# Kernel tuning notes

Measured on AMD Instinct MI355X. Metric: run time of the kernel, lower is better.

The kernel has to match this reference:

```python
import jax, jax.numpy as jnp
import numpy as np

D = 200; K = 10; NHEAD = 5; HDIM = 40; ANS = 2; THRESH = 0.4; GHEAD = 5; GC = 2
B = 8; L = 80; R = 64

def _lin(x, W, b):
    return x @ W + b

def _ln(x, g, b):
    m = jnp.mean(x, -1, keepdims=True)
    v = jnp.var(x, -1, keepdims=True)
    return (x - m) / jnp.sqrt(v + 1e-5) * g + b

def _sparsemax(z):
    # sparsemax along last axis (Martins & Astudillo)
    zs = -jnp.sort(-z, axis=-1)
    k = jnp.arange(1, z.shape[-1] + 1, dtype=z.dtype)
    cs = jnp.cumsum(zs, -1)
    supp = jnp.sum((1.0 + k * zs) > cs, -1, keepdims=True)
    tau = (jnp.take_along_axis(cs, supp - 1, -1) - 1.0) / supp.astype(z.dtype)
    return jnp.maximum(z - tau, 0.0)

def _pair(a, b):
    # a [B,n,d], b [B,m,d] -> [B,n*m,4d] feature cat [a, b, a*b, a-b]
    Bn, n, d = a.shape; m = b.shape[1]
    a1 = jnp.broadcast_to(a[:, :, None, :], (Bn, n, m, d))
    b1 = jnp.broadcast_to(b[:, None, :, :], (Bn, n, m, d))
    return jnp.concatenate([a1, b1, a1 * b1, a1 - b1], -1).reshape(Bn, n * m, 4 * d)

def _topk_sel(E, s, mask):
    # select top-K instances by score (masked)
    s = jnp.where(mask, s, -jnp.inf)
    _, idx = jax.lax.top_k(s, K)
    return jnp.take_along_axis(E, idx[:, :, None], axis=1)

def _mco(x, W_attn, b_attn, W_ff1, b_ff1, W_ff2, b_ff2, ln_g, ln_b):
    # transformer encoder layer: MHA + FFN, post-norm (dropout off at eval)
    Bn, N, d = x.shape
    q = _lin(x, W_attn[0], b_attn[0]).reshape(Bn, N, NHEAD, HDIM)
    k = _lin(x, W_attn[1], b_attn[1]).reshape(Bn, N, NHEAD, HDIM)
    v = _lin(x, W_attn[2], b_attn[2]).reshape(Bn, N, NHEAD, HDIM)
    att = jax.nn.softmax(jnp.einsum('bnhk,bmhk->bhnm', q, k) / np.float32(np.sqrt(HDIM)), axis=-1)
    o = jnp.einsum('bhnm,bmhk->bnhk', att, v).reshape(Bn, N, d)
    x = _ln(x + _lin(o, W_attn[3], b_attn[3]), ln_g[0], ln_b[0])
    f = _lin(jax.nn.relu(_lin(x, W_ff1, b_ff1)), W_ff2, b_ff2)
    return _ln(x + f, ln_g[1], ln_b[1])

def _forward(imgs, encoded_texts, mask_T, mask_TT, mask_TV, adj,
             answer_set, Wt, bt, Wi1, bi1, Wi2, bi2, Wgc, bgc, Wps, bps, Wts, bts,
             W_single, b_single, W_pair1, b_pair1, W_pair2, b_pair2, W_topk, b_topk,
             clues, W_clue1, b_clue1, W_ans1, b_ans1, W_inst2, b_inst2, W_ans2, b_ans2,
             W_attn, b_attn, W_ff1, b_ff1, W_ff2, b_ff2, ln_g, ln_b,
             W_guide, b_guide, W_at1, b_at1, W_at2, b_at2):
    imgs_0 = jax.nn.relu(_lin(jax.nn.relu(_lin(imgs, Wi1, bi1)), Wi2, bi2))  # ImageEncoder 768->500->200
    texts_0 = _lin(encoded_texts, Wt, bt)                                    # TextEncoder 768->200
    Bn, l, _ = texts_0.shape
    r = imgs_0.shape[1]
    ones_V = jnp.ones((Bn, r), bool)
    ones_VV = jnp.ones((Bn, r * r), bool)
    out = []
    for gc_i in range(GC):
        def pair_mlp(f, i):
            return jax.nn.relu(_lin(jax.nn.relu(_lin(f, W_pair1[i], b_pair1[i])), W_pair2[i], b_pair2[i]))
        def score(E, i):
            return jax.nn.relu(E @ W_topk[i] + b_topk[i])
        # five modality streams
        E_T = jax.nn.relu(_lin(texts_0, W_single[0], b_single[0]))
        E_V = jax.nn.relu(_lin(imgs_0, W_single[1], b_single[1]))
        E_TT = pair_mlp(_pair(texts_0, texts_0), 0)
        E_TV = pair_mlp(_pair(texts_0, imgs_0), 1)
        E_VV = pair_mlp(_pair(imgs_0, imgs_0), 2)
        E_T_k = _topk_sel(E_T, score(E_T, 0), mask_T)
        E_V_k = _topk_sel(E_V, score(E_V, 1), ones_V)
        E_TT_k = _topk_sel(E_TT, score(E_TT, 2), mask_TT)
        E_TV_k = _topk_sel(E_TV, score(E_TV, 3), mask_TV)
        E_VV_k = _topk_sel(E_VV, score(E_VV, 4), ones_VV)
        # clue binding: attend selected instances onto per-stream clue banks, condition on answer set
        ans1 = _lin(answer_set, W_ans1, b_ans1)
        def bind(Ek, c):
            att = jax.nn.softmax(jnp.einsum('bkd,cd->bkc', Ek, c), -1)
            bound = jnp.einsum('bkc,cd->bkd', att, c)
            return jax.nn.relu(_lin(bound, W_clue1, b_clue1)[:, :, None, :] + ans1[None, None])
        preds = jnp.concatenate([bind(E_T_k, clues[0]), bind(E_V_k, clues[1]), bind(E_TT_k, clues[2]), bind(E_TV_k, clues[3]), bind(E_VV_k, clues[4])], axis=1)  # [B,5K,A,D]
        E_cat = jnp.concatenate([E_T_k, E_V_k, E_TT_k, E_TV_k, E_VV_k], 1)
        E4 = jnp.broadcast_to(E_cat[:, :, None, :], preds.shape)
        inst_score = jnp.einsum('bnad,ad->bna', _lin(E4, W_inst2, b_inst2), _lin(answer_set, W_ans2, b_ans2))
        preds_ = jnp.stack([_mco(preds[:, :, a, :], W_attn, b_attn, W_ff1, b_ff1, W_ff2, b_ff2, ln_g, ln_b) for a in range(ANS)], axis=2)
        feat = jnp.concatenate([E4, preds, E4 - preds, E4 * preds], -1)
        atoms = jax.nn.sigmoid(_lin(jax.nn.relu(_lin(feat, W_at1, b_at1)), W_at2, b_at2))[..., 0]
        atoms = jnp.transpose(atoms, (2, 0, 1))  # [A,B,5K]
        # global text/image embeddings for guide scores
        I_score = jax.nn.softmax(imgs_0 @ Wps + bps, -1)
        T_score = jax.nn.softmax(texts_0 @ Wts + bts, -1)
        I_emb = jnp.einsum('brd,br->bd', imgs_0, I_score)
        T_emb = jnp.einsum('bld,bl->bd', texts_0, T_score)
        E_IT = pair_mlp(jnp.concatenate([T_emb, I_emb, T_emb * I_emb, T_emb - I_emb], -1), 1)
        heads = []
        for gi in range(GHEAD):
            g1 = jnp.einsum('bnad,d->bna', preds_, W_guide[2 * gi]) + b_guide[2 * gi]
            g2 = (E_IT @ W_guide[2 * gi + 1] + b_guide[2 * gi + 1])[:, None, None]
            fcs = _sparsemax(g1 * g2) * _sparsemax(inst_score)
            fcs = _sparsemax(jnp.transpose(fcs, (2, 0, 1)))  # [A,B,5K], sparsemax over instances
            flag = fcs >= THRESH
            mprod = jnp.prod(jnp.where(flag, atoms, 1.0), -1)  # conjunction over selected atoms
            vals, idx = jax.lax.top_k(fcs, 3)                  # fallback: top-3 atoms weighted by score
            fb = jnp.prod(jnp.take_along_axis(atoms, idx, -1) * vals, -1)
            heads.append(jnp.where(jnp.any(flag, -1), mprod, fb))  # [A,B]
        out.append(jnp.max(jnp.stack(heads, -1), -1))  # max over guide heads -> [A,B]
        # graph convolution refines text+image node features for next iteration
        graph = jnp.concatenate([texts_0, imgs_0], 1)
        graph = jax.nn.relu(jnp.einsum('bnm,bmd->bnd', adj, graph) @ Wgc[gc_i] + bgc[gc_i])
        texts_0 = graph[:, :l, :]
        imgs_0 = graph[:, l:, :]
    return jnp.stack(out)  # [GC, A, B]

def setup_inputs():
    ks = jax.random.split(jax.random.key(0), 64)
    def rn(i, shape, s=0.05):
        return jax.random.normal(ks[i], shape, dtype=jnp.float32) * s
    inp = {}
    inp['imgs'] = rn(0, (B, R, 768), 1.0)
    inp['encoded_texts'] = rn(1, (B, L, 768), 1.0)
    inp['mask_batch_T'] = jnp.ones((B, L), dtype=bool)
    inp['mask_batch_TT'] = jnp.ones((B, L * L), dtype=bool)
    inp['mask_batch_TV'] = jnp.ones((B, L * R), dtype=bool)
    inp['adj_matrix'] = jax.random.uniform(ks[2], (B, L + R, L + R), dtype=jnp.float32) / (L + R)
    inp['word_len'] = jax.random.randint(ks[3], (B,), 1, L)
    inp['word_spans'] = jax.random.randint(ks[4], (B, L, 2), 0, L)
    inp['answer_set'] = rn(5, (ANS, D), 0.5)
    inp['Wt'] = rn(6, (768, D)); inp['bt'] = rn(7, (D,))
    inp['Wi1'] = rn(8, (768, 500)); inp['bi1'] = rn(9, (500,))
    inp['Wi2'] = rn(10, (500, D)); inp['bi2'] = rn(11, (D,))
    inp['Wgc'] = rn(12, (GC, D, D)); inp['bgc'] = rn(13, (GC, D))
    inp['Wps'] = rn(14, (D,), 0.5); inp['bps'] = rn(15, ())
    inp['Wts'] = rn(16, (D,), 0.5); inp['bts'] = rn(17, ())
    inp['W_single'] = rn(18, (2, D, D)); inp['b_single'] = rn(19, (2, D))
    inp['W_pair1'] = rn(20, (3, 4 * D, 2 * D)); inp['b_pair1'] = rn(21, (3, 2 * D))
    inp['W_pair2'] = rn(22, (3, 2 * D, D)); inp['b_pair2'] = rn(23, (3, D))
    inp['W_topk'] = rn(24, (5, D), 0.5); inp['b_topk'] = rn(25, (5,))
    inp['clues'] = rn(26, (5, 5, D), 0.5)
    inp['W_clue1'] = rn(27, (D, D)); inp['b_clue1'] = rn(28, (D,))
    inp['W_ans1'] = rn(29, (D, D)); inp['b_ans1'] = rn(30, (D,))
    inp['W_inst2'] = rn(31, (D, D)); inp['b_inst2'] = rn(32, (D,))
    inp['W_ans2'] = rn(33, (D, D)); inp['b_ans2'] = rn(34, (D,))
    inp['W_attn'] = rn(35, (4, D, D)); inp['b_attn'] = rn(36, (4, D))
    inp['W_ff1'] = rn(37, (D, 2 * D)); inp['b_ff1'] = rn(38, (2 * D,))
    inp['W_ff2'] = rn(39, (2 * D, D)); inp['b_ff2'] = rn(40, (D,))
    inp['ln_g'] = jnp.ones((2, D), jnp.float32); inp['ln_b'] = jnp.zeros((2, D), jnp.float32)
    inp['W_guide'] = rn(41, (2 * GHEAD, D), 0.5); inp['b_guide'] = rn(42, (2 * GHEAD,))
    inp['W_at1'] = rn(43, (4 * D, 2 * D)); inp['b_at1'] = rn(44, (2 * D,))
    inp['W_at2'] = rn(45, (2 * D, 1)); inp['b_at2'] = rn(46, (1,))
    return inp

def reference(imgs, encoded_texts, mask_batch_T, mask_batch_TT, mask_batch_TV, adj_matrix, word_len, word_spans,
              answer_set, Wt, bt, Wi1, bi1, Wi2, bi2, Wgc, bgc, Wps, bps, Wts, bts,
              W_single, b_single, W_pair1, b_pair1, W_pair2, b_pair2, W_topk, b_topk,
              clues, W_clue1, b_clue1, W_ans1, b_ans1, W_inst2, b_inst2, W_ans2, b_ans2,
              W_attn, b_attn, W_ff1, b_ff1, W_ff2, b_ff2, ln_g, ln_b,
              W_guide, b_guide, W_at1, b_at1, W_at2, b_at2):
    # word_len / word_spans are consumed by the (simplified) TextEncoder pooling; not needed here
    return _forward(imgs, encoded_texts, mask_batch_T, mask_batch_TT, mask_batch_TV, adj_matrix,
                    answer_set, Wt, bt, Wi1, bi1, Wi2, bi2, Wgc, bgc, Wps, bps, Wts, bts,
                    W_single, b_single, W_pair1, b_pair1, W_pair2, b_pair2, W_topk, b_topk,
                    clues, W_clue1, b_clue1, W_ans1, b_ans1, W_inst2, b_inst2, W_ans2, b_ans2,
                    W_attn, b_attn, W_ff1, b_ff1, W_ff2, b_ff2, ln_g, ln_b,
                    W_guide, b_guide, W_at1, b_at1, W_at2, b_at2)
```

## Files before the change

kernel.cpp:

```cpp
#include <hip/hip_runtime.h>
#include <hip/hip_bf16.h>


__device__ __forceinline__ void sparsemax2(float z0, float z1, float& o0, float& o1) {
  float S0 = (z1 > z0) ? z1 : 0.f;
  float S1 = (z0 > z1) ? z0 : 0.f;
  float cz0 = (z1 > z0) ? z0 : 0.f;
  float cz1 = (z0 > z1) ? z1 : 0.f;
  bool c0 = (1.f + cz0) > S0;
  bool c1 = (1.f + cz1) > S1;
  float supp = (c0 ? 1.f : 0.f) + (c1 ? 1.f : 0.f);
  float Ss   = (c0 ? z0  : 0.f) + (c1 ? z1  : 0.f);
  float tau = (Ss - 1.f) / supp;
  o0 = fmaxf(z0 - tau, 0.f);
  o1 = fmaxf(z1 - tau, 0.f);
}

__global__ __launch_bounds__(256) void gemm_k(
    const float* __restrict__ A, const float* __restrict__ Bw,
    const float* __restrict__ bias, float* __restrict__ C,
    int M, int N, int K, long sA, long sB, long sC, int act)
{
  int batch = blockIdx.z;
  A  += (long)batch * sA;
  Bw += (long)batch * sB;
  C  += (long)batch * sC;
  __shared__ float As[32][33];
  __shared__ float Bs[32][33];
  int tid = threadIdx.x;
  int tx = tid & 15, ty = tid >> 4;
  int row0 = blockIdx.y * 32, col0 = blockIdx.x * 32;
  float acc00 = 0.f, acc01 = 0.f, acc10 = 0.f, acc11 = 0.f;
  for (int k0 = 0; k0 < K; k0 += 32) {
    for (int i = tid; i < 1024; i += 256) {
      int r = i >> 5, c = i & 31;
      int ar = row0 + r, ac = k0 + c;
      As[r][c] = (ar < M && ac < K) ? A[(long)ar * K + ac] : 0.f;
      int br = k0 + r, bc = col0 + c;
      Bs[r][c] = (br < K && bc < N) ? Bw[(long)br * N + bc] : 0.f;
    }
    __syncthreads();
#pragma unroll
    for (int kk = 0; kk < 32; ++kk) {
      float a0 = As[ty * 2][kk], a1 = As[ty * 2 + 1][kk];
      float b0 = Bs[kk][tx * 2], b1 = Bs[kk][tx * 2 + 1];
      acc00 += a0 * b0; acc01 += a0 * b1; acc10 += a1 * b0; acc11 += a1 * b1;
    }
    __syncthreads();
  }
  int r0 = row0 + ty * 2, c0 = col0 + tx * 2;
#define STORE_(rr, cc, v)                                        \
  if ((rr) < M && (cc) < N) {                                    \
    float t_ = (v) + (bias ? bias[cc] : 0.f);                    \
    if (act) t_ = fmaxf(t_, 0.f);                                \
    C[(long)(rr) * N + (cc)] = t_;                               \
  }
  STORE_(r0, c0, acc00); STORE_(r0, c0 + 1, acc01);
  STORE_(r0 + 1, c0, acc10); STORE_(r0 + 1, c0 + 1, acc11);
#undef STORE_
}

__global__ void wab_kernel(const float* __restrict__ P1, float* __restrict__ Wa,
                           float* __restrict__ Wb) {
  int idx = blockIdx.x * 256 + threadIdx.x;
  if (idx >= 240000) return;
  int t = idx / 80000, r2 = idx % 80000;
  int d = r2 / 400, k = r2 % 400;
  long base = (long)t * 320000;
  float wd = P1[base + (long)(600 + d) * 400 + k];
  Wa[idx] = P1[base + (long)d * 400 + k] + wd;
  Wb[idx] = P1[base + (long)(200 + d) * 400 + k] - wd;
}

__global__ void repack_kernel(const float* __restrict__ W_pair1,
                              const float* __restrict__ W_pair2,
                              float* __restrict__ Wcq, float* __restrict__ W2q) {
  int idx = blockIdx.x * 256 + threadIdx.x;
  if (idx < 259200) {
    int t = idx / 86400, r = idx % 86400;
    int dc = r / 1728, r2 = r % 1728;
    int tk = r2 / 108, m = r2 % 108;
    int j = m >> 2, dd = m & 3;
    const float* Wc = W_pair1 + (long)t * 320000 + 160000;
    Wcq[idx] = (j < 25) ? Wc[(long)(dc * 4 + dd) * 400 + tk * 25 + j] : 0.f;
  } else if (idx < 518400) {
    int id2 = idx - 259200;
    int t = id2 / 86400, r = id2 % 86400;
    int kc = r / 864, r2 = r % 864;
    int c8 = r2 / 108, m = r2 % 108;
    int j = m >> 2, kk = m & 3;
    const float* W2 = W_pair2 + (long)t * 80000;
    W2q[id2] = (j < 25) ? W2[(long)(kc * 4 + kk) * 200 + c8 * 25 + j] : 0.f;
  }
}

__global__ void ans_kernel(const float* __restrict__ as, const float* __restrict__ W1,
                           const float* __restrict__ b1, const float* __restrict__ W2,
                           const float* __restrict__ b2, float* __restrict__ ans1,
                           float* __restrict__ ans2) {
  int idx = blockIdx.x * 256 + threadIdx.x;
  if (idx >= 400) return;
  int a = idx / 200, d = idx % 200;
  float a1 = b1[d], a2 = b2[d];
  for (int k = 0; k < 200; ++k) {
    float av = as[a * 200 + k];
    a1 += av * W1[k * 200 + d];
    a2 += av * W2[k * 200 + d];
  }
  ans1[idx] = a1;
  ans2[idx] = a2;
}

__global__ void rowdot_kernel(const float* __restrict__ E, const float* __restrict__ Wt,
                              const float* __restrict__ bt, int g, float* __restrict__ s,
                              int rows) {
  int r = blockIdx.x * 256 + threadIdx.x;
  if (r >= rows) return;
  const float* e = E + (long)r * 200;
  const float* w = Wt + g * 200;
  float acc = bt[g];
  for (int d = 0; d < 200; ++d) acc += e[d] * w[d];
  s[r] = fmaxf(acc, 0.f);
}

__global__ __launch_bounds__(256) void pair_score_kernel(
    const float* __restrict__ Arows, int an, const float* __restrict__ Brows, int bm,
    const float* __restrict__ At, const float* __restrict__ Bt,
    const float* __restrict__ Wcq, const float* __restrict__ W2q,
    const float* __restrict__ b2, const float* __restrict__ wt,
    const float* __restrict__ btk, int gidx, float* __restrict__ scores)
{
  const int tid = threadIdx.x;
  const int b = blockIdx.y;
  const int nTJ = bm >> 2;
  const int i0 = (blockIdx.x / nTJ) * 8;
  const int j0 = (blockIdx.x % nTJ) * 4;

  Arows += (long)b * an * 200;
  Brows += (long)b * bm * 200;
  At += (long)b * an * 400;
  Bt += (long)b * bm * 400;
  scores += (long)b * an * bm;

  __shared__ __align__(16) float smem[12800];
  __shared__ __align__(16) float stg[3456];

  const int tq = tid >> 4;
  const int tk = tid & 15;
  const int tp8 = tid >> 3;
  const int tc8 = tid & 7;

  for (int idx = tid; idx < 6400; idx += 256) {
    int p = idx / 200, d = idx - p * 200;
    smem[p * 200 + d] = Arows[(long)(i0 + (p >> 2)) * 200 + d] *
                        Brows[(long)(j0 + (p & 3)) * 200 + d];
  }

  {
    const float4* src = reinterpret_cast<const float4*>(Wcq);
    float4* dst = reinterpret_cast<float4*>(stg);
#pragma unroll
    for (int l = 0; l < 2; ++l) {
      int idx = tid + l * 256;
      if (idx < 432) dst[idx] = src[idx];
    }
  }
  __syncthreads();

  float acc[2][25];
#pragma unroll
  for (int q = 0; q < 2; ++q)
#pragma unroll
    for (int j = 0; j < 25; ++j) acc[q][j] = 0.f;

  for (int ph = 0; ph < 50; ++ph) {
    const int cur = ph & 1, nxt = cur ^ 1;
    float4 pre[2];
    if (ph < 49) {
      const float4* src = reinterpret_cast<const float4*>(Wcq) + (ph + 1) * 432;
#pragma unroll
      for (int l = 0; l < 2; ++l) {
        int idx = tid + l * 256;
        pre[l] = (idx < 432) ? src[idx] : make_float4(0.f, 0.f, 0.f, 0.f);
      }
    }
    const float4* pd4 = reinterpret_cast<const float4*>(smem);
    const float4 p0 = pd4[(2 * tq + 0) * 50 + ph];
    const float4 p1 = pd4[(2 * tq + 1) * 50 + ph];
    const float4* wb = reinterpret_cast<const float4*>(stg) + cur * 432 + tk * 27;
#pragma unroll
    for (int j = 0; j < 25; ++j) {
      const float4 w = wb[j];
      float a0 = acc[0][j], a1 = acc[1][j];
      a0 = fmaf(p0.x, w.x, a0); a1 = fmaf(p1.x, w.x, a1);
      a0 = fmaf(p0.y, w.y, a0); a1 = fmaf(p1.y, w.y, a1);
      a0 = fmaf(p0.z, w.z, a0); a1 = fmaf(p1.z, w.z, a1);
      a0 = fmaf(p0.w, w.w, a0); a1 = fmaf(p1.w, w.w, a1);
      acc[0][j] = a0; acc[1][j] = a1;
    }
    if (ph < 49) {
      float4* dst = reinterpret_cast<float4*>(stg) + nxt * 432;
#pragma unroll
      for (int l = 0; l < 2; ++l) {
        int idx = tid + l * 256;
        if (idx < 432) dst[idx] = pre[l];
      }
    }
    __syncthreads();
  }

  {
    const float* Ar = &At[(long)(i0 + (tq >> 1)) * 400 + tk * 25];
#pragma unroll
    for (int q = 0; q < 2; ++q) {
      const float* Br = &Bt[(long)(j0 + ((2 * tq + q) & 3)) * 400 + tk * 25];
#pragma unroll
      for (int j = 0; j < 25; ++j)
        acc[q][j] = fmaxf(acc[q][j] + Ar[j] + Br[j], 0.f);
    }
  }

#pragma unroll
  for (int q = 0; q < 2; ++q)
#pragma unroll
    for (int j = 0; j < 25; ++j)
      smem[(2 * tq + q) * 400 + tk * 25 + j] = acc[q][j];
  {
    const float4* src = reinterpret_cast<const float4*>(W2q);
    float4* dst = reinterpret_cast<float4*>(stg);
#pragma unroll
    for (int l = 0; l < 2; ++l) {
      int idx = tid + l * 256;
      if (idx < 432) dst[idx] = src[idx];
    }
  }
  __syncthreads();

  float acc2[25];
#pragma unroll
  for (int j = 0; j < 25; ++j) acc2[j] = 0.f;

  for (int ph = 0; ph < 50; ++ph) {
    const int cur = ph & 1, nxt = cur ^ 1;
    float4 pre[2];
    if (ph < 49) {
      const float4* src = reinterpret_cast<const float4*>(W2q) + (ph + 1) * 432;
#pragma unroll
      for (int l = 0; l < 2; ++l) {
        int idx = tid + l * 256;
        pre[l] = (idx < 432) ? src[idx] : make_float4(0.f, 0.f, 0.f, 0.f);
      }
    }
    const float4* H4 = reinterpret_cast<const float4*>(smem);
#pragma unroll
    for (int gg = 0; gg < 2; ++gg) {
      const int kc = ph * 2 + gg;
      const float4 h = H4[tp8 * 100 + kc];
      const float4* wb =
          reinterpret_cast<const float4*>(stg) + cur * 432 + gg * 216 + tc8 * 27;
#pragma unroll
      for (int j = 0; j < 25; ++j) {
        const float4 w = wb[j];
        float a = acc2[j];
        a = fmaf(h.x, w.x, a);
        a = fmaf(h.y, w.y, a);
        a = fmaf(h.z, w.z, a);
        a = fmaf(h.w, w.w, a);
        acc2[j] = a;
      }
    }
    if (ph < 49) {
      float4* dst = reinterpret_cast<float4*>(stg) + nxt * 432;
#pragma unroll
      for (int l = 0; l < 2; ++l) {
        int idx = tid + l * 256;
        if (idx < 432) dst[idx] = pre[l];
      }
    }
    __syncthreads();
  }

  float part = 0.f;
#pragma unroll
  for (int j = 0; j < 25; ++j) {
    const int c = tc8 * 25 + j;
    part += fmaxf(acc2[j] + b2[c], 0.f) * wt[c];
  }
#pragma unroll
  for (int off = 1; off < 8; off <<= 1) part += __shfl_xor(part, off, 64);
  if ((tid & 7) == 0) {
    const int p = tp8;
    scores[(long)(i0 + (p >> 2)) * bm + (j0 + (p & 3))] =
        fmaxf(part + btk[gidx], 0.f);
  }
}

__global__ void topk_kernel(const float* __restrict__ sT, const float* __restrict__ sV,
                            const float* __restrict__ sTT, const float* __restrict__ sTV,
                            const float* __restrict__ sVV, int* __restrict__ topIdx) {
  int g = blockIdx.x, b = blockIdx.y, tid = threadIdx.x;
  const float* src; int len;
  switch (g) {
    case 0: src = sT + b * 80; len = 80; break;
    case 1: src = sV + b * 64; len = 64; break;
    case 2: src = sTT + b * 6400; len = 6400; break;
    case 3: src = sTV + b * 5120; len = 5120; break;
    default: src = sVV + b * 4096; len = 4096; break;
  }
  __shared__ float sbuf[6400];
  __shared__ float rv[256];
  __shared__ int ri[256];
  for (int i = tid; i < len; i += 256) sbuf[i] = src[i];
  __syncthreads();
  for (int r = 0; r < 10; ++r) {
    float bv = -1e30f; int bi = 0x7fffffff;
    for (int i = tid; i < len; i += 256) {
      float v = sbuf[i];
      if (v > bv) { bv = v; bi = i; }
    }
    rv[tid] = bv; ri[tid] = bi;
    __syncthreads();
    for (int s = 128; s > 0; s >>= 1) {
      if (tid < s) {
        if (rv[tid + s] > rv[tid] || (rv[tid + s] == rv[tid] && ri[tid + s] < ri[tid])) {
          rv[tid] = rv[tid + s]; ri[tid] = ri[tid + s];
        }
      }
      __syncthreads();
    }
    if (tid == 0) {
      topIdx[(g * 8 + b) * 10 + r] = ri[0];
      sbuf[ri[0]] = -1e30f;
    }
    __syncthreads();
  }
}

__global__ void gather_kernel(
    const int* __restrict__ topIdx, const float* __restrict__ ETf,
    const float* __restrict__ EVf, const float* __restrict__ texts0,
    const float* __restrict__ imgs0, const float* __restrict__ AtTT,
    const float* __restrict__ BtTT, const float* __restrict__ AtTV,
    const float* __restrict__ BtTV, const float* __restrict__ AtVV,
    const float* __restrict__ BtVV, const float* __restrict__ W_pair1,
    const float* __restrict__ W_pair2, const float* __restrict__ b_pair2,
    float* __restrict__ E_cat)
{
  int n = blockIdx.x, b = blockIdx.y, tid = threadIdx.x;
  int g = n / 10, r = n % 10;
  int idx = topIdx[(g * 8 + b) * 10 + r];
  float* out = E_cat + ((long)(b * 50 + n)) * 200;
  if (g == 0) {
    for (int d = tid; d < 200; d += 256) out[d] = ETf[((long)(b * 80 + idx)) * 200 + d];
    return;
  }
  if (g == 1) {
    for (int d = tid; d < 200; d += 256) out[d] = EVf[((long)(b * 64 + idx)) * 200 + d];
    return;
  }
  int t = g - 2;
  int m = (t == 0) ? 80 : 64;
  int i = idx / m, j = idx % m;
  const float* ar = (t == 2) ? imgs0 + ((long)(b * 64 + i)) * 200
                             : texts0 + ((long)(b * 80 + i)) * 200;
  const float* br = (t == 0) ? texts0 + ((long)(b * 80 + j)) * 200
                             : imgs0 + ((long)(b * 64 + j)) * 200;
  const float* Atp = ((t == 0) ? AtTT : (t == 1) ? AtTV : AtVV) +
                     ((long)(b * ((t == 2) ? 64 : 80) + i)) * 400;
  const float* Btp = ((t == 0) ? BtTT : (t == 1) ? BtTV : BtVV) +
                     ((long)(b * ((t == 0) ? 80 : 64) + j)) * 400;
  const float* Wc = W_pair1 + (long)t * 320000 + 160000;
  const float* W2 = W_pair2 + (long)t * 80000;
  const float* bb2 = b_pair2 + t * 200;
  __shared__ float pd[200];
  __shared__ float hh[400];
  for (int d = tid; d < 200; d += 256) pd[d] = ar[d] * br[d];
  __syncthreads();
  for (int k = tid; k < 400; k += 256) {
    float acc = Atp[k] + Btp[k];
    for (int d = 0; d < 200; ++d) acc += pd[d] * Wc[(long)d * 400 + k];
    hh[k] = fmaxf(acc, 0.f);
  }
  __syncthreads();
  for (int c = tid; c < 200; c += 256) {
    float acc = bb2[c];
    for (int k = 0; k < 400; ++k) acc += hh[k] * W2[(long)k * 200 + c];
    out[c] = fmaxf(acc, 0.f);
  }
}

__global__ void bind_kernel(const float* __restrict__ E_cat, const float* __restrict__ clues,
                            const float* __restrict__ W_clue1, const float* __restrict__ b_clue1,
                            const float* __restrict__ ans1, const float* __restrict__ W_inst2,
                            const float* __restrict__ b_inst2, const float* __restrict__ ans2,
                            float* __restrict__ preds, float* __restrict__ inst) {
  int n = blockIdx.x, b = blockIdx.y, tid = threadIdx.x;
  int g = n / 10;
  const float* e = E_cat + ((long)(b * 50 + n)) * 200;
  __shared__ float es[200], att[5], bound[200], vv[200], red[256];
  for (int d = tid; d < 200; d += 256) es[d] = e[d];
  __syncthreads();
  if (tid < 5) {
    const float* cl = clues + ((long)(g * 5 + tid)) * 200;
    float acc = 0.f;
    for (int d = 0; d < 200; ++d) acc += es[d] * cl[d];
    att[tid] = acc;
  }
  __syncthreads();
  if (tid == 0) {
    float mx = att[0];
    for (int c = 1; c < 5; ++c) mx = fmaxf(mx, att[c]);
    float s = 0.f;
    for (int c = 0; c < 5; ++c) { att[c] = expf(att[c] - mx); s += att[c]; }
    float inv = 1.f / s;
    for (int c = 0; c < 5; ++c) att[c] *= inv;
  }
  __syncthreads();
  if (tid < 200) {
    float acc = 0.f;
    for (int c = 0; c < 5; ++c) acc += att[c] * clues[((long)(g * 5 + c)) * 200 + tid];
    bound[tid] = acc;
  }
  __syncthreads();
  if (tid < 200) {
    float acc = b_clue1[tid];
    for (int k = 0; k < 200; ++k) acc += bound[k] * W_clue1[(long)k * 200 + tid];
    long rbase = ((long)(b * 50 + n)) * 2;
    preds[(rbase + 0) * 200 + tid] = fmaxf(acc + ans1[tid], 0.f);
    preds[(rbase + 1) * 200 + tid] = fmaxf(acc + ans1[200 + tid], 0.f);
    float a2 = b_inst2[tid];
    for (int k = 0; k < 200; ++k) a2 += es[k] * W_inst2[(long)k * 200 + tid];
    vv[tid] = a2;
  }
  __syncthreads();
  float p0 = 0.f, p1 = 0.f;
  for (int d = tid; d < 200; d += 256) {
    p0 += vv[d] * ans2[d];
    p1 += vv[d] * ans2[200 + d];
  }
  red[tid] = p0; __syncthreads();
  for (int s = 128; s > 0; s >>= 1) { if (tid < s) red[tid] += red[tid + s]; __syncthreads(); }
  if (tid == 0) inst[((long)(b * 50 + n)) * 2 + 0] = red[0];
  __syncthreads();
  red[tid] = p1; __syncthreads();
  for (int s = 128; s > 0; s >>= 1) { if (tid < s) red[tid] += red[tid + s]; __syncthreads(); }
  if (tid == 0) inst[((long)(b * 50 + n)) * 2 + 1] = red[0];
// ... 200 lines not shown
    }
    __syncthreads();
    if (tid < 100) {
      int a = tid / 50, n = tid % 50;
      fcs[a][n] = fmaxf(fcs1[n][a] - tau[a], 0.f);
    }
    __syncthreads();
    if (tid < 2) {
      int a = tid;
      bool anyF = false;
      float mp = 1.f;
      for (int n = 0; n < 50; ++n) {
        if (fcs[a][n] >= 0.4f) { anyF = true; mp *= atm[n][a]; }
      }
      int p0 = -1, p1 = -1;
      float fb = 1.f;
      for (int t3 = 0; t3 < 3; ++t3) {
        float bv = -1e30f; int bi = -1;
        for (int n = 0; n < 50; ++n) {
          if (n == p0 || n == p1) continue;
          float v = fcs[a][n];
          if (v > bv) { bv = v; bi = n; }
        }
        if (t3 == 0) p0 = bi; else if (t3 == 1) p1 = bi;
        fb *= atm[bi][a] * bv;
      }
      float head = anyF ? mp : fb;
      hm[a] = fmaxf(hm[a], head);
    }
    __syncthreads();
  }
  if (tid < 2) dout[gc * 16 + tid * 8 + b] = hm[tid];
}

__global__ void graph_pack(const float* __restrict__ texts0, const float* __restrict__ imgs0,
                           float* __restrict__ gin) {
  int row = blockIdx.x, tid = threadIdx.x;
  int b = row / 144, rr = row % 144;
  const float* src = (rr < 80) ? texts0 + ((long)(b * 80 + rr)) * 200
                               : imgs0 + ((long)(b * 64 + rr - 80)) * 200;
  float* dst = gin + (long)row * 200;
  if (tid < 200) dst[tid] = src[tid];
}

__global__ void graph_unpack(const float* __restrict__ gout, float* __restrict__ texts0,
                             float* __restrict__ imgs0) {
  int row = blockIdx.x, tid = threadIdx.x;
  int b = row / 144, rr = row % 144;
  const float* src = gout + (long)row * 200;
  float* dst = (rr < 80) ? texts0 + ((long)(b * 80 + rr)) * 200
                         : imgs0 + ((long)(b * 64 + rr - 80)) * 200;
  if (tid < 200) dst[tid] = src[tid];
}

extern "C" void kernel_launch(void* const* d_in, const int* in_sizes, int n_in,
                              void* d_out, int out_size, void* d_ws, size_t ws_size,
                              hipStream_t stream) {
  (void)in_sizes; (void)n_in; (void)out_size; (void)ws_size;
  const float* imgs = (const float*)d_in[0];
  const float* etexts = (const float*)d_in[1];
  const float* adj = (const float*)d_in[5];
  const float* answer_set = (const float*)d_in[8];
  const float* Wt = (const float*)d_in[9];
  const float* bt = (const float*)d_in[10];
  const float* Wi1 = (const float*)d_in[11];
  const float* bi1 = (const float*)d_in[12];
  const float* Wi2 = (const float*)d_in[13];
  const float* bi2 = (const float*)d_in[14];
  const float* Wgc = (const float*)d_in[15];
  const float* bgc = (const float*)d_in[16];
  const float* Wps = (const float*)d_in[17];
  const float* bps = (const float*)d_in[18];
  const float* Wts = (const float*)d_in[19];
  const float* bts = (const float*)d_in[20];
  const float* W_single = (const float*)d_in[21];
  const float* b_single = (const float*)d_in[22];
  const float* W_pair1 = (const float*)d_in[23];
  const float* b_pair1 = (const float*)d_in[24];
  const float* W_pair2 = (const float*)d_in[25];
  const float* b_pair2 = (const float*)d_in[26];
  const float* W_topk = (const float*)d_in[27];
  const float* b_topk = (const float*)d_in[28];
  const float* clues = (const float*)d_in[29];
  const float* W_clue1 = (const float*)d_in[30];
  const float* b_clue1 = (const float*)d_in[31];
  const float* W_ans1 = (const float*)d_in[32];
  const float* b_ans1 = (const float*)d_in[33];
  const float* W_inst2 = (const float*)d_in[34];
  const float* b_inst2 = (const float*)d_in[35];
  const float* W_ans2 = (const float*)d_in[36];
  const float* b_ans2 = (const float*)d_in[37];
  const float* W_attn = (const float*)d_in[38];
  const float* b_attn = (const float*)d_in[39];
  const float* W_ff1 = (const float*)d_in[40];
  const float* b_ff1 = (const float*)d_in[41];
  const float* W_ff2 = (const float*)d_in[42];
  const float* b_ff2 = (const float*)d_in[43];
  const float* ln_g = (const float*)d_in[44];
  const float* ln_b = (const float*)d_in[45];
  const float* W_guide = (const float*)d_in[46];
  const float* b_guide = (const float*)d_in[47];
  const float* W_at1 = (const float*)d_in[48];
  const float* b_at1 = (const float*)d_in[49];
  const float* W_at2 = (const float*)d_in[50];
  const float* b_at2 = (const float*)d_in[51];

  float* W = (float*)d_ws;
  size_t off = 0;
  auto A_ = [&](size_t n) { float* p = W + off; off += n; return p; };
  float* texts0 = A_(128000);
  float* imgs0 = A_(102400);
  float* tmp500 = A_(256000);
  float* Wa = A_(240000);
  float* Wb = A_(240000);
  float* Wcq = A_(259200);
  float* W2q = A_(259200);
  float* AtTT = A_(256000);
  float* BtTT = A_(256000);
  float* AtTV = A_(256000);
  float* BtTV = A_(204800);
  float* AtVV = A_(204800);
  float* BtVV = A_(204800);
  float* ETf = A_(128000);
  float* EVf = A_(102400);
  float* sT = A_(640);
  float* sV = A_(512);
  float* sTT = A_(51200);
  float* sTV = A_(40960);
  float* sVV = A_(32768);
  float* E_cat = A_(80000);
  float* ans1 = A_(400);
  float* ans2 = A_(400);
  float* preds = A_(160000);
  float* inst = A_(800);
  float* bufQ = A_(160000);
  float* bufK = A_(160000);
  float* bufV = A_(160000);
  float* bufO = A_(160000);
  float* bufT1 = A_(160000);
  float* bufX1 = A_(160000);
  float* bufF1 = A_(320000);
  float* bufF2 = A_(160000);
  float* predsM = A_(160000);
  float* featb = A_(640000);
  float* bufAt = A_(320000);
  float* atoms = A_(800);
  float* E_IT = A_(1600);
  float* gin = A_(230400);
  float* tmpG = A_(230400);
  float* gout = A_(230400);
  int* topIdx = (int*)A_(400);

  dim3 blk(256);
  auto launch_gemm = [&](const float* Aa, const float* Bb, const float* bias, float* C,
                         int M, int N, int K, int act, int batch = 1, long sA = 0,
                         long sB = 0, long sC = 0) {
    dim3 g((N + 31) / 32, (M + 31) / 32, batch);
    gemm_k<<<g, blk, 0, stream>>>(Aa, Bb, bias, C, M, N, K, sA, sB, sC, act);
  };

  launch_gemm(imgs, Wi1, bi1, tmp500, 512, 500, 768, 1);
  launch_gemm(tmp500, Wi2, bi2, imgs0, 512, 200, 500, 1);
  launch_gemm(etexts, Wt, bt, texts0, 640, 200, 768, 0);
  wab_kernel<<<(240000 + 255) / 256, blk, 0, stream>>>(W_pair1, Wa, Wb);
  repack_kernel<<<(518400 + 255) / 256, blk, 0, stream>>>(W_pair1, W_pair2, Wcq, W2q);
  ans_kernel<<<2, blk, 0, stream>>>(answer_set, W_ans1, b_ans1, W_ans2, b_ans2, ans1, ans2);

  for (int gc = 0; gc < 2; ++gc) {
    launch_gemm(texts0, W_single, b_single, ETf, 640, 200, 200, 1);
    launch_gemm(imgs0, W_single + 40000, b_single + 200, EVf, 512, 200, 200, 1);
    rowdot_kernel<<<3, blk, 0, stream>>>(ETf, W_topk, b_topk, 0, sT, 640);
    rowdot_kernel<<<2, blk, 0, stream>>>(EVf, W_topk, b_topk, 1, sV, 512);
    launch_gemm(texts0, Wa, nullptr, AtTT, 640, 400, 200, 0);
    launch_gemm(texts0, Wb, b_pair1, BtTT, 640, 400, 200, 0);
    launch_gemm(texts0, Wa + 80000, nullptr, AtTV, 640, 400, 200, 0);
    launch_gemm(imgs0, Wb + 80000, b_pair1 + 400, BtTV, 512, 400, 200, 0);
    launch_gemm(imgs0, Wa + 160000, nullptr, AtVV, 512, 400, 200, 0);
    launch_gemm(imgs0, Wb + 160000, b_pair1 + 800, BtVV, 512, 400, 200, 0);
    pair_score_kernel<<<dim3(200, 8), blk, 0, stream>>>(
        texts0, 80, texts0, 80, AtTT, BtTT, Wcq, W2q, b_pair2,
        W_topk + 400, b_topk, 2, sTT);
    pair_score_kernel<<<dim3(160, 8), blk, 0, stream>>>(
        texts0, 80, imgs0, 64, AtTV, BtTV, Wcq + 86400, W2q + 86400,
        b_pair2 + 200, W_topk + 600, b_topk, 3, sTV);
    pair_score_kernel<<<dim3(128, 8), blk, 0, stream>>>(
        imgs0, 64, imgs0, 64, AtVV, BtVV, Wcq + 172800, W2q + 172800,
        b_pair2 + 400, W_topk + 800, b_topk, 4, sVV);
    topk_kernel<<<dim3(5, 8), blk, 0, stream>>>(sT, sV, sTT, sTV, sVV, topIdx);
    gather_kernel<<<dim3(50, 8), blk, 0, stream>>>(topIdx, ETf, EVf, texts0, imgs0, AtTT,
                                                   BtTT, AtTV, BtTV, AtVV, BtVV, W_pair1,
                                                   W_pair2, b_pair2, E_cat);
    bind_kernel<<<dim3(50, 8), blk, 0, stream>>>(E_cat, clues, W_clue1, b_clue1, ans1,
                                                 W_inst2, b_inst2, ans2, preds, inst);
    launch_gemm(preds, W_attn, b_attn, bufQ, 800, 200, 200, 0);
    launch_gemm(preds, W_attn + 40000, b_attn + 200, bufK, 800, 200, 200, 0);
    launch_gemm(preds, W_attn + 80000, b_attn + 400, bufV, 800, 200, 200, 0);
    attn_kernel<<<dim3(5, 2, 8), blk, 0, stream>>>(bufQ, bufK, bufV, bufO);
    launch_gemm(bufO, W_attn + 120000, b_attn + 600, bufT1, 800, 200, 200, 0);
    ln_kernel<<<800, blk, 0, stream>>>(preds, bufT1, ln_g, ln_b, bufX1);
    launch_gemm(bufX1, W_ff1, b_ff1, bufF1, 800, 400, 200, 1);
    launch_gemm(bufF1, W_ff2, b_ff2, bufF2, 800, 200, 400, 0);
    ln_kernel<<<800, blk, 0, stream>>>(bufX1, bufF2, ln_g + 200, ln_b + 200, predsM);
    feat_kernel<<<800, blk, 0, stream>>>(E_cat, preds, featb);
    launch_gemm(featb, W_at1, b_at1, bufAt, 800, 400, 800, 1);
    atoms_kernel<<<800, blk, 0, stream>>>(bufAt, W_at2, b_at2, atoms);
    emb_kernel<<<8, blk, 0, stream>>>(texts0, imgs0, Wts, bts, Wps, bps, W_pair1, b_pair1,
                                      W_pair2, b_pair2, E_IT);
    head_kernel<<<8, blk, 0, stream>>>(predsM, inst, atoms, E_IT, W_guide, b_guide,
                                       (float*)d_out, gc);
    if (gc == 0) {
      graph_pack<<<1152, blk, 0, stream>>>(texts0, imgs0, gin);
      launch_gemm(adj, gin, nullptr, tmpG, 144, 200, 144, 0, 8, 144 * 144, 144 * 200,
                  144 * 200);
      launch_gemm(tmpG, Wgc, bgc, gout, 1152, 200, 200, 1);
      graph_unpack<<<1152, blk, 0, stream>>>(gout, texts0, imgs0);
    }
  }
}
```

Before: 4.712 ms.

## Double pair tile per block in pair_score and split second GEMM into halves

Each pair_score block now handles 8x8 pairs instead of 8x4. Every thread accumulates four pair rows in the first GEMM and two in the second, so each staged weight element is reused across twice as many pairs, and the grid is halved. The hidden activations are written to shared memory in two swizzled halves so that the 64-pair by 400 hidden tile fits in the existing buffer. The cost is higher register pressure (acc grows to 100 floats), which may reduce occupancy or spill, and fewer blocks to fill the GPU.

```diff
diff --git a/kernel.cpp b/kernel.cpp
--- a/kernel.cpp
+++ b/kernel.cpp
@@ -132,9 +132,9 @@
 {
   const int tid = threadIdx.x;
   const int b = blockIdx.y;
-  const int nTJ = bm >> 2;
+  const int nTJ = bm >> 3;
   const int i0 = (blockIdx.x / nTJ) * 8;
-  const int j0 = (blockIdx.x % nTJ) * 4;
+  const int j0 = (blockIdx.x % nTJ) * 8;
 
   Arows += (long)b * an * 200;
   Brows += (long)b * bm * 200;
@@ -145,153 +145,164 @@
   __shared__ __align__(16) float smem[12800];
   __shared__ __align__(16) float stg[3456];
 
-  const int tq = tid >> 4;
+  const int tp = tid >> 4;
   const int tk = tid & 15;
-  const int tp8 = tid >> 3;
+  const int u = tid >> 3;
   const int tc8 = tid & 7;
 
-  for (int idx = tid; idx < 6400; idx += 256) {
+  for (int idx = tid; idx < 12800; idx += 256) {
     int p = idx / 200, d = idx - p * 200;
-    smem[p * 200 + d] = Arows[(long)(i0 + (p >> 2)) * 200 + d] *
-                        Brows[(long)(j0 + (p & 3)) * 200 + d];
+    smem[p * 200 + d] = Arows[(long)(i0 + (p >> 3)) * 200 + d] *
+                        Brows[(long)(j0 + (p & 7)) * 200 + d];
   }
 
   {
     const float4* src = reinterpret_cast<const float4*>(Wcq);
     float4* dst = reinterpret_cast<float4*>(stg);
-#pragma unroll
-    for (int l = 0; l < 2; ++l) {
-      int idx = tid + l * 256;
-      if (idx < 432) dst[idx] = src[idx];
-    }
-  }
-  __syncthreads();
-
-  float acc[2][25];
-#pragma unroll
-  for (int q = 0; q < 2; ++q)
+    dst[tid] = src[tid];
+    if (tid < 176) dst[256 + tid] = src[256 + tid];
+  }
+  __syncthreads();
+
+  float acc[4][25];
+#pragma unroll
+  for (int q = 0; q < 4; ++q)
 #pragma unroll
     for (int j = 0; j < 25; ++j) acc[q][j] = 0.f;
 
   for (int ph = 0; ph < 50; ++ph) {
     const int cur = ph & 1, nxt = cur ^ 1;
-    float4 pre[2];
+    float4 pre0, pre1;
     if (ph < 49) {
       const float4* src = reinterpret_cast<const float4*>(Wcq) + (ph + 1) * 432;
-#pragma unroll
-      for (int l = 0; l < 2; ++l) {
-        int idx = tid + l * 256;
-        pre[l] = (idx < 432) ? src[idx] : make_float4(0.f, 0.f, 0.f, 0.f);
-      }
+      pre0 = src[tid];
+      pre1 = (tid < 176) ? src[256 + tid] : make_float4(0.f, 0.f, 0.f, 0.f);
     }
     const float4* pd4 = reinterpret_cast<const float4*>(smem);
-    const float4 p0 = pd4[(2 * tq + 0) * 50 + ph];
-    const float4 p1 = pd4[(2 * tq + 1) * 50 + ph];
+    float4 pq[4];
+#pragma unroll
+    for (int q = 0; q < 4; ++q) pq[q] = pd4[(tp * 4 + q) * 50 + ph];
     const float4* wb = reinterpret_cast<const float4*>(stg) + cur * 432 + tk * 27;
 #pragma unroll
     for (int j = 0; j < 25; ++j) {
       const float4 w = wb[j];
-      float a0 = acc[0][j], a1 = acc[1][j];
-      a0 = fmaf(p0.x, w.x, a0); a1 = fmaf(p1.x, w.x, a1);
-      a0 = fmaf(p0.y, w.y, a0); a1 = fmaf(p1.y, w.y, a1);
-      a0 = fmaf(p0.z, w.z, a0); a1 = fmaf(p1.z, w.z, a1);
-      a0 = fmaf(p0.w, w.w, a0); a1 = fmaf(p1.w, w.w, a1);
-      acc[0][j] = a0; acc[1][j] = a1;
+#pragma unroll
+      for (int q = 0; q < 4; ++q) {
+        float a = acc[q][j];
+        a = fmaf(pq[q].x, w.x, a);
+        a = fmaf(pq[q].y, w.y, a);
+        a = fmaf(pq[q].z, w.z, a);
+        a = fmaf(pq[q].w, w.w, a);
+        acc[q][j] = a;
+      }
     }
     if (ph < 49) {
       float4* dst = reinterpret_cast<float4*>(stg) + nxt * 432;
-#pragma unroll
-      for (int l = 0; l < 2; ++l) {
-        int idx = tid + l * 256;
-        if (idx < 432) dst[idx] = pre[l];
-      }
+      dst[tid] = pre0;
+      if (tid < 176) dst[256 + tid] = pre1;
     }
     __syncthreads();
   }
 
   {
-    const float* Ar = &At[(long)(i0 + (tq >> 1)) * 400 + tk * 25];
-#pragma unroll
-    for (int q = 0; q < 2; ++q) {
-      const float* Br = &Bt[(long)(j0 + ((2 * tq + q) & 3)) * 400 + tk * 25];
+    const float* Ar = &At[(long)(i0 + (tp >> 1)) * 400 + tk * 25];
+#pragma unroll
+    for (int q = 0; q < 4; ++q) {
+      const float* Br = &Bt[(long)(j0 + (tp & 1) * 4 + q) * 400 + tk * 25];
 #pragma unroll
       for (int j = 0; j < 25; ++j)
         acc[q][j] = fmaxf(acc[q][j] + Ar[j] + Br[j], 0.f);
     }
   }
 
+  float acc2[2][25];
 #pragma unroll
   for (int q = 0; q < 2; ++q)
 #pragma unroll
-    for (int j = 0; j < 25; ++j)
-      smem[(2 * tq + q) * 400 + tk * 25 + j] = acc[q][j];
-  {
-    const float4* src = reinterpret_cast<const float4*>(W2q);
-    float4* dst = reinterpret_cast<float4*>(stg);
-#pragma unroll
-    for (int l = 0; l < 2; ++l) {
-      int idx = tid + l * 256;
-      if (idx < 432) dst[idx] = src[idx];
-    }
-  }
-  __syncthreads();
-
-  float acc2[25];
-#pragma unroll
-  for (int j = 0; j < 25; ++j) acc2[j] = 0.f;
-
-  for (int ph = 0; ph < 50; ++ph) {
-    const int cur = ph & 1, nxt = cur ^ 1;
-    float4 pre[2];
-    if (ph < 49) {
-      const float4* src = reinterpret_cast<const float4*>(W2q) + (ph + 1) * 432;
-#pragma unroll
-      for (int l = 0; l < 2; ++l) {
-        int idx = tid + l * 256;
-        pre[l] = (idx < 432) ? src[idx] : make_float4(0.f, 0.f, 0.f, 0.f);
+    for (int j = 0; j < 25; ++j) acc2[q][j] = 0.f;
+
+  float4* const H4 = reinterpret_cast<float4*>(smem);
+
+  for (int P = 0; P < 2; ++P) {
+    if ((tk >> 3) == P) {
+      const int klbase = (tk & 7) * 25;
+#pragma unroll
+      for (int j = 0; j < 25; ++j) {
+        const int kl = klbase + j;
+        H4[kl * 16 + (tp ^ ((kl & 7) * 2))] =
+            make_float4(acc[0][j], acc[1][j], acc[2][j], acc[3][j]);
       }
     }
-    const float4* H4 = reinterpret_cast<const float4*>(smem);
-#pragma unroll
-    for (int gg = 0; gg < 2; ++gg) {
-      const int kc = ph * 2 + gg;
-      const float4 h = H4[tp8 * 100 + kc];
-      const float4* wb =
-          reinterpret_cast<const float4*>(stg) + cur * 432 + gg * 216 + tc8 * 27;
-#pragma unroll
-      for (int j = 0; j < 25; ++j) {
-        const float4 w = wb[j];
-        float a = acc2[j];
-        a = fmaf(h.x, w.x, a);
-        a = fmaf(h.y, w.y, a);
-        a = fmaf(h.z, w.z, a);
-        a = fmaf(h.w, w.w, a);
-        acc2[j] = a;
+    {
+      const float4* src = reinterpret_cast<const float4*>(W2q) + (P * 50) * 216;
+      float4* dst = reinterpret_cast<float4*>(stg);
+      dst[tid] = src[tid];
+      if (tid < 176) dst[256 + tid] = src[256 + tid];
+    }
+    __syncthreads();
+
+    for (int ph = 0; ph < 25; ++ph) {
+      const int cur = ph & 1, nxt = cur ^ 1;
+      float4 pre0, pre1;
+      if (ph < 24) {
+        const float4* src =
+            reinterpret_cast<const float4*>(W2q) + (P * 50 + (ph + 1) * 2) * 216;
+        pre0 = src[tid];
+        pre1 = (tid < 176) ? src[256 + tid] : make_float4(0.f, 0.f, 0.f, 0.f);
       }
-    }
-    if (ph < 49) {
-      float4* dst = reinterpret_cast<float4*>(stg) + nxt * 432;
-#pragma unroll
-      for (int l = 0; l < 2; ++l) {
-        int idx = tid + l * 256;
-        if (idx < 432) dst[idx] = pre[l];
+#pragma unroll
+      for (int gg = 0; gg < 2; ++gg) {
+        const int klbase = (ph * 2 + gg) * 4;
+        float2 h[4];
+#pragma unroll
+        for (int kk = 0; kk < 4; ++kk) {
+          const int kl = klbase + kk;
+          const int c4 = (u >> 1) ^ ((kl & 7) * 2);
+          h[kk] = *reinterpret_cast<const float2*>(
+              &smem[kl * 64 + c4 * 4 + (u & 1) * 2]);
+        }
+        const float4* wb =
+            reinterpret_cast<const float4*>(stg) + cur * 432 + gg * 216 + tc8 * 27;
+#pragma unroll
+        for (int j = 0; j < 25; ++j) {
+          const float4 w = wb[j];
+          float a0 = acc2[0][j], a1 = acc2[1][j];
+          a0 = fmaf(h[0].x, w.x, a0); a1 = fmaf(h[0].y, w.x, a1);
+          a0 = fmaf(h[1].x, w.y, a0); a1 = fmaf(h[1].y, w.y, a1);
+          a0 = fmaf(h[2].x, w.z, a0); a1 = fmaf(h[2].y, w.z, a1);
+          a0 = fmaf(h[3].x, w.w, a0); a1 = fmaf(h[3].y, w.w, a1);
+          acc2[0][j] = a0; acc2[1][j] = a1;
+        }
       }
-    }
-    __syncthreads();
-  }
-
-  float part = 0.f;
+      if (ph < 24) {
+        float4* dst = reinterpret_cast<float4*>(stg) + nxt * 432;
+        dst[tid] = pre0;
+        if (tid < 176) dst[256 + tid] = pre1;
+      }
+      __syncthreads();
+    }
+  }
+
+  float part[2] = {0.f, 0.f};
 #pragma unroll
   for (int j = 0; j < 25; ++j) {
     const int c = tc8 * 25 + j;
-    part += fmaxf(acc2[j] + b2[c], 0.f) * wt[c];
-  }
-#pragma unroll
-  for (int off = 1; off < 8; off <<= 1) part += __shfl_xor(part, off, 64);
+    const float bb = b2[c], ww = wt[c];
+    part[0] += fmaxf(acc2[0][j] + bb, 0.f) * ww;
+    part[1] += fmaxf(acc2[1][j] + bb, 0.f) * ww;
+  }
+#pragma unroll
+  for (int off = 1; off < 8; off <<= 1) {
+    part[0] += __shfl_xor(part[0], off, 64);
+    part[1] += __shfl_xor(part[1], off, 64);
+  }
   if ((tid & 7) == 0) {
-    const int p = tp8;
-    scores[(long)(i0 + (p >> 2)) * bm + (j0 + (p & 3))] =
-        fmaxf(part + btk[gidx], 0.f);
+    const float bt_ = btk[gidx];
+#pragma unroll
+    for (int q = 0; q < 2; ++q) {
+      const int p = 2 * u + q;
+      scores[(long)(i0 + (p >> 3)) * bm + (j0 + (p & 7))] = fmaxf(part[q] + bt_, 0.f);
+    }
   }
 }
 
@@ -823,13 +834,13 @@
     launch_gemm(imgs0, Wb + 80000, b_pair1 + 400, BtTV, 512, 400, 200, 0);
     launch_gemm(imgs0, Wa + 160000, nullptr, AtVV, 512, 400, 200, 0);
     launch_gemm(imgs0, Wb + 160000, b_pair1 + 800, BtVV, 512, 400, 200, 0);
-    pair_score_kernel<<<dim3(200, 8), blk, 0, stream>>>(
+    pair_score_kernel<<<dim3(100, 8), blk, 0, stream>>>(
         texts0, 80, texts0, 80, AtTT, BtTT, Wcq, W2q, b_pair2,
         W_topk + 400, b_topk, 2, sTT);
-    pair_score_kernel<<<dim3(160, 8), blk, 0, stream>>>(
+    pair_score_kernel<<<dim3(80, 8), blk, 0, stream>>>(
         texts0, 80, imgs0, 64, AtTV, BtTV, Wcq + 86400, W2q + 86400,
         b_pair2 + 200, W_topk + 600, b_topk, 3, sTV);
-    pair_score_kernel<<<dim3(128, 8), blk, 0, stream>>>(
+    pair_score_kernel<<<dim3(64, 8), blk, 0, stream>>>(
         imgs0, 64, imgs0, 64, AtVV, BtVV, Wcq + 172800, W2q + 172800,
         b_pair2 + 400, W_topk + 800, b_topk, 4, sVV);
     topk_kernel<<<dim3(5, 8), blk, 0, stream>>>(sT, sV, sTT, sTV, sVV, topIdx);
```

Result: faster. 4.264 ms (-9.5%).

## Double pair tile per block in pair_score kernel to halve weight streaming

Applied to the files above, without the earlier changes.

Each pair_score block now covers an 8x8 pair tile with 512 threads instead of an 8x4 tile with 256, so every staged Wcq/W2q chunk serves twice as many pairs and total weight traffic from global memory is halved. The hidden activations for the second GEMM no longer fit in shared memory at once. They are written in two halves into a swizzled, transposed layout and the second GEMM runs as two passes. This adds extra barriers, raises shared-memory and register pressure per block, and halves the number of blocks launched.

```diff
diff --git a/kernel.cpp b/kernel.cpp
--- a/kernel.cpp
+++ b/kernel.cpp
@@ -123,7 +123,7 @@
   s[r] = fmaxf(acc, 0.f);
 }
 
-__global__ __launch_bounds__(256) void pair_score_kernel(
+__global__ __launch_bounds__(512) void pair_score_kernel(
     const float* __restrict__ Arows, int an, const float* __restrict__ Brows, int bm,
     const float* __restrict__ At, const float* __restrict__ Bt,
     const float* __restrict__ Wcq, const float* __restrict__ W2q,
@@ -132,9 +132,9 @@
 {
   const int tid = threadIdx.x;
   const int b = blockIdx.y;
-  const int nTJ = bm >> 2;
+  const int nTJ = bm >> 3;
   const int i0 = (blockIdx.x / nTJ) * 8;
-  const int j0 = (blockIdx.x % nTJ) * 4;
+  const int j0 = (blockIdx.x % nTJ) * 8;
 
   Arows += (long)b * an * 200;
   Brows += (long)b * bm * 200;
@@ -147,23 +147,17 @@
 
   const int tq = tid >> 4;
   const int tk = tid & 15;
-  const int tp8 = tid >> 3;
+  const int u = tid >> 3;
   const int tc8 = tid & 7;
 
-  for (int idx = tid; idx < 6400; idx += 256) {
+  for (int idx = tid; idx < 12800; idx += 512) {
     int p = idx / 200, d = idx - p * 200;
-    smem[p * 200 + d] = Arows[(long)(i0 + (p >> 2)) * 200 + d] *
-                        Brows[(long)(j0 + (p & 3)) * 200 + d];
-  }
-
-  {
-    const float4* src = reinterpret_cast<const float4*>(Wcq);
-    float4* dst = reinterpret_cast<float4*>(stg);
-#pragma unroll
-    for (int l = 0; l < 2; ++l) {
-      int idx = tid + l * 256;
-      if (idx < 432) dst[idx] = src[idx];
-    }
+    smem[p * 200 + d] = Arows[(long)(i0 + (p >> 3)) * 200 + d] *
+                        Brows[(long)(j0 + (p & 7)) * 200 + d];
+  }
+
+  if (tid < 432) {
+    reinterpret_cast<float4*>(stg)[tid] = reinterpret_cast<const float4*>(Wcq)[tid];
   }
   __syncthreads();
 
@@ -175,15 +169,9 @@
 
   for (int ph = 0; ph < 50; ++ph) {
     const int cur = ph & 1, nxt = cur ^ 1;
-    float4 pre[2];
-    if (ph < 49) {
-      const float4* src = reinterpret_cast<const float4*>(Wcq) + (ph + 1) * 432;
-#pragma unroll
-      for (int l = 0; l < 2; ++l) {
-        int idx = tid + l * 256;
-        pre[l] = (idx < 432) ? src[idx] : make_float4(0.f, 0.f, 0.f, 0.f);
-      }
-    }
+    float4 pre0;
+    if (ph < 49 && tid < 432)
+      pre0 = (reinterpret_cast<const float4*>(Wcq) + (ph + 1) * 432)[tid];
     const float4* pd4 = reinterpret_cast<const float4*>(smem);
     const float4 p0 = pd4[(2 * tq + 0) * 50 + ph];
     const float4 p1 = pd4[(2 * tq + 1) * 50 + ph];
@@ -198,86 +186,76 @@
       a0 = fmaf(p0.w, w.w, a0); a1 = fmaf(p1.w, w.w, a1);
       acc[0][j] = a0; acc[1][j] = a1;
     }
-    if (ph < 49) {
-      float4* dst = reinterpret_cast<float4*>(stg) + nxt * 432;
-#pragma unroll
-      for (int l = 0; l < 2; ++l) {
-        int idx = tid + l * 256;
-        if (idx < 432) dst[idx] = pre[l];
-      }
-    }
+    if (ph < 49 && tid < 432)
+      (reinterpret_cast<float4*>(stg) + nxt * 432)[tid] = pre0;
     __syncthreads();
   }
 
   {
-    const float* Ar = &At[(long)(i0 + (tq >> 1)) * 400 + tk * 25];
+    const float* Ar = &At[(long)(i0 + (tq >> 2)) * 400 + tk * 25];
 #pragma unroll
     for (int q = 0; q < 2; ++q) {
-      const float* Br = &Bt[(long)(j0 + ((2 * tq + q) & 3)) * 400 + tk * 25];
+      const float* Br = &Bt[(long)(j0 + ((2 * tq + q) & 7)) * 400 + tk * 25];
 #pragma unroll
       for (int j = 0; j < 25; ++j)
         acc[q][j] = fmaxf(acc[q][j] + Ar[j] + Br[j], 0.f);
     }
   }
 
-#pragma unroll
-  for (int q = 0; q < 2; ++q)
-#pragma unroll
-    for (int j = 0; j < 25; ++j)
-      smem[(2 * tq + q) * 400 + tk * 25 + j] = acc[q][j];
-  {
-    const float4* src = reinterpret_cast<const float4*>(W2q);
-    float4* dst = reinterpret_cast<float4*>(stg);
-#pragma unroll
-    for (int l = 0; l < 2; ++l) {
-      int idx = tid + l * 256;
-      if (idx < 432) dst[idx] = src[idx];
-    }
-  }
-  __syncthreads();
-
   float acc2[25];
 #pragma unroll
   for (int j = 0; j < 25; ++j) acc2[j] = 0.f;
 
-  for (int ph = 0; ph < 50; ++ph) {
-    const int cur = ph & 1, nxt = cur ^ 1;
-    float4 pre[2];
-    if (ph < 49) {
-      const float4* src = reinterpret_cast<const float4*>(W2q) + (ph + 1) * 432;
-#pragma unroll
-      for (int l = 0; l < 2; ++l) {
-        int idx = tid + l * 256;
-        pre[l] = (idx < 432) ? src[idx] : make_float4(0.f, 0.f, 0.f, 0.f);
+  for (int P = 0; P < 2; ++P) {
+    if ((tk >> 3) == P) {
+      const int klbase = (tk & 7) * 25;
+#pragma unroll
+      for (int j = 0; j < 25; ++j) {
+        const int kl = klbase + j;
+        const int c2 = tq ^ ((kl & 7) << 2);
+        *reinterpret_cast<float2*>(&smem[kl * 64 + c2 * 2]) =
+            make_float2(acc[0][j], acc[1][j]);
       }
     }
-    const float4* H4 = reinterpret_cast<const float4*>(smem);
-#pragma unroll
-    for (int gg = 0; gg < 2; ++gg) {
-      const int kc = ph * 2 + gg;
-      const float4 h = H4[tp8 * 100 + kc];
-      const float4* wb =
-          reinterpret_cast<const float4*>(stg) + cur * 432 + gg * 216 + tc8 * 27;
-#pragma unroll
-      for (int j = 0; j < 25; ++j) {
-        const float4 w = wb[j];
-        float a = acc2[j];
-        a = fmaf(h.x, w.x, a);
-        a = fmaf(h.y, w.y, a);
-        a = fmaf(h.z, w.z, a);
-        a = fmaf(h.w, w.w, a);
-        acc2[j] = a;
+    if (tid < 432) {
+      reinterpret_cast<float4*>(stg)[tid] =
+          (reinterpret_cast<const float4*>(W2q) + (P * 50) * 216)[tid];
+    }
+    __syncthreads();
+
+    for (int ph = 0; ph < 25; ++ph) {
+      const int cur = ph & 1, nxt = cur ^ 1;
+      float4 pre0;
+      if (ph < 24 && tid < 432)
+        pre0 = (reinterpret_cast<const float4*>(W2q) +
+                (P * 50 + (ph + 1) * 2) * 216)[tid];
+#pragma unroll
+      for (int gg = 0; gg < 2; ++gg) {
+        const int klbase = (ph * 2 + gg) * 4;
+        float h[4];
+#pragma unroll
+        for (int kk = 0; kk < 4; ++kk) {
+          const int kl = klbase + kk;
+          const int c2 = (u >> 1) ^ ((kl & 7) << 2);
+          h[kk] = smem[kl * 64 + c2 * 2 + (u & 1)];
+        }
+        const float4* wb =
+            reinterpret_cast<const float4*>(stg) + cur * 432 + gg * 216 + tc8 * 27;
+#pragma unroll
+        for (int j = 0; j < 25; ++j) {
+          const float4 w = wb[j];
+          float a = acc2[j];
+          a = fmaf(h[0], w.x, a);
+          a = fmaf(h[1], w.y, a);
+          a = fmaf(h[2], w.z, a);
+          a = fmaf(h[3], w.w, a);
+          acc2[j] = a;
+        }
       }
-    }
-    if (ph < 49) {
-      float4* dst = reinterpret_cast<float4*>(stg) + nxt * 432;
-#pragma unroll
-      for (int l = 0; l < 2; ++l) {
-        int idx = tid + l * 256;
-        if (idx < 432) dst[idx] = pre[l];
-      }
-    }
-    __syncthreads();
+      if (ph < 24 && tid < 432)
+        (reinterpret_cast<float4*>(stg) + nxt * 432)[tid] = pre0;
+      __syncthreads();
+    }
   }
 
   float part = 0.f;
@@ -289,8 +267,7 @@
 #pragma unroll
   for (int off = 1; off < 8; off <<= 1) part += __shfl_xor(part, off, 64);
   if ((tid & 7) == 0) {
-    const int p = tp8;
-    scores[(long)(i0 + (p >> 2)) * bm + (j0 + (p & 3))] =
+    scores[(long)(i0 + (u >> 3)) * bm + (j0 + (u & 7))] =
         fmaxf(part + btk[gidx], 0.f);
   }
 }
@@ -798,6 +775,7 @@
   int* topIdx = (int*)A_(400);
 
   dim3 blk(256);
+  dim3 blk512(512);
   auto launch_gemm = [&](const float* Aa, const float* Bb, const float* bias, float* C,
                          int M, int N, int K, int act, int batch = 1, long sA = 0,
                          long sB = 0, long sC = 0) {
@@ -823,13 +801,13 @@
     launch_gemm(imgs0, Wb + 80000, b_pair1 + 400, BtTV, 512, 400, 200, 0);
     launch_gemm(imgs0, Wa + 160000, nullptr, AtVV, 512, 400, 200, 0);
     launch_gemm(imgs0, Wb + 160000, b_pair1 + 800, BtVV, 512, 400, 200, 0);
-    pair_score_kernel<<<dim3(200, 8), blk, 0, stream>>>(
+    pair_score_kernel<<<dim3(100, 8), blk512, 0, stream>>>(
         texts0, 80, texts0, 80, AtTT, BtTT, Wcq, W2q, b_pair2,
         W_topk + 400, b_topk, 2, sTT);
-    pair_score_kernel<<<dim3(160, 8), blk, 0, stream>>>(
+    pair_score_kernel<<<dim3(80, 8), blk512, 0, stream>>>(
         texts0, 80, imgs0, 64, AtTV, BtTV, Wcq + 86400, W2q + 86400,
         b_pair2 + 200, W_topk + 600, b_topk, 3, sTV);
-    pair_score_kernel<<<dim3(128, 8), blk, 0, stream>>>(
+    pair_score_kernel<<<dim3(64, 8), blk512, 0, stream>>>(
         imgs0, 64, imgs0, 64, AtVV, BtVV, Wcq + 172800, W2q + 172800,
         b_pair2 + 400, W_topk + 800, b_topk, 4, sVV);
     topk_kernel<<<dim3(5, 8), blk, 0, stream>>>(sT, sV, sTT, sTV, sVV, topIdx);
```

After: 4.504 ms. 1.05x faster.
